# Kernel optimization log

Hardware: AMD Instinct MI355X
Metric: run time of the kernel (lower is better)

The kernel has to match this reference:

```python
import jax, jax.numpy as jnp
import numpy as np

FACTOR = 2  # upsample factor per spatial dim


def setup_inputs() -> dict:
    key = jax.random.key(0)
    k1, k2, k3 = jax.random.split(key, 3)
    B, C_in, C_out, H, W_ = 8, 128, 128, 64, 64
    x = jax.random.normal(k1, (B, C_in, H, W_), dtype=jnp.float32)
    # conv3x3 params (OIHW), fan-in scaled init like torch Conv2d default scale
    fan_in = C_in * 3 * 3
    W = jax.random.normal(k2, (C_out, C_in, 3, 3), dtype=jnp.float32) / np.sqrt(fan_in)
    b = jax.random.normal(k3, (C_out,), dtype=jnp.float32) * 0.01
    return {"x": x, "W": W, "b": b}


def reference(x, W, b):
    h = jnp.repeat(jnp.repeat(x, FACTOR, axis=2), FACTOR, axis=3)  # [B,C,2H,2W]
    # conv3x3: stride 1, padding 1
    out = jax.lax.conv_general_dilated(
        h, W,
        window_strides=(1, 1),
        padding=((1, 1), (1, 1)),
        dimension_numbers=("NCHW", "OIHW", "NCHW"),
    )
    return out + b[None, :, None, None]
```

## Files before the change

kernel.cpp:

```cpp
#include <hip/hip_runtime.h>
#include <stdint.h>

typedef short bf16x8 __attribute__((ext_vector_type(8)));
typedef float f32x4 __attribute__((ext_vector_type(4)));

#define NCI 128
#define NCO 128
#define HIN 64
#define HP  66
#define NB  8

__device__ __forceinline__ unsigned short f32_to_bf16(float f) {
    union { float f; uint32_t u; } v; v.f = f;
    return (unsigned short)((v.u + 0x7FFFu + ((v.u >> 16) & 1u)) >> 16);
}

__device__ __forceinline__ void gl_lds16(const void* g, void* l) {
    __builtin_amdgcn_global_load_lds(
        (const __attribute__((address_space(1))) unsigned int*)g,
        (__attribute__((address_space(3))) unsigned int*)l, 16, 0, 0);
}

__device__ __forceinline__ void vmw0() {
    asm volatile("s_waitcnt vmcnt(0)" ::: "memory");
}
__device__ __forceinline__ void lkw0() {
    asm volatile("s_waitcnt lgkmcnt(0)" ::: "memory");
}
__device__ __forceinline__ void barx() {
    asm volatile("" ::: "memory");
    __builtin_amdgcn_s_barrier();
    asm volatile("" ::: "memory");
}

__device__ __forceinline__ float weff_sum(const float* wp, int py, int px, int ty, int tx) {
    float s = 0.f;
    #pragma unroll
    for (int ky = 0; ky < 3; ++ky) {
        bool iy = (py == 0) ? (ty == 0 ? (ky == 0) : (ky >= 1))
                            : (ty == 0 ? (ky <= 1) : (ky == 2));
        if (!iy) continue;
        #pragma unroll
        for (int kx = 0; kx < 3; ++kx) {
            bool ix = (px == 0) ? (tx == 0 ? (kx == 0) : (kx >= 1))
                                : (tx == 0 ? (kx <= 1) : (kx == 2));
            if (ix) s += wp[ky * 3 + kx];
        }
    }
    return s;
}

__global__ __launch_bounds__(256) void prep_kernel(
        const float* __restrict__ W, const float* __restrict__ x,
        unsigned short* __restrict__ Aw5, unsigned short* __restrict__ xq) {
    if (blockIdx.x < 1024) {
        int idx = blockIdx.x * 256 + threadIdx.x;
        int e   = idx & 7;
        int rl  = (idx >> 3) & 15;
        int pl  = (idx >> 7) & 3;
        int f   = (idx >> 9) & 3;
        int wm  = (idx >> 11) & 1;
        int kt  = (idx >> 12) & 15;
        int par = idx >> 16;
        int co = wm * 64 + f * 16 + rl;
        int k  = kt * 32 + pl * 8 + e;
        int tap = k >> 7, ci = k & 127;
        Aw5[idx] = f32_to_bf16(weff_sum(W + (co * NCI + ci) * 9,
                                        par >> 1, par & 1, tap >> 1, tap & 1));
    } else {
        const int bb = blockIdx.x - 1024;
        const int b = bb / HP, hp = bb % HP;
        const int t = threadIdx.x;
        if (hp == 0 || hp == HP - 1) {
            bf16x8 z = (bf16x8){0, 0, 0, 0, 0, 0, 0, 0};
            for (int i = t; i < 4 * HP * 4; i += 256) {
                int g = i / (HP * 4), rem = i % (HP * 4);
                unsigned short* dst = xq +
                    ((((size_t)(b * 4 + g) * HP + hp) * HP) << 5) + rem * 8;
                *(bf16x8*)dst = z;
            }
            return;
        }
        const int h = hp - 1;
        if (t < 32) {
            bf16x8 z = (bf16x8){0, 0, 0, 0, 0, 0, 0, 0};
            int g = t >> 3, wpc = ((t >> 2) & 1) * (HP - 1), q = t & 3;
            unsigned short* dst = xq +
                ((((size_t)(b * 4 + g) * HP + hp) * HP + wpc) << 5) + q * 8;
            *(bf16x8*)dst = z;
        }
        const int w = t & 63, g = t >> 6;
        const float* src = x + ((size_t)(b * NCI + g * 32) * (HIN * HIN)) + h * HIN + w;
        unsigned short* dst = xq +
            ((((size_t)(b * 4 + g) * HP + hp) * HP + (w + 1)) << 5);
        #pragma unroll
        for (int q = 0; q < 4; ++q) {
            bf16x8 v;
            #pragma unroll
            for (int j = 0; j < 8; ++j)
                v[j] = (short)f32_to_bf16(src[(size_t)(q * 8 + j) * (HIN * HIN)]);
            *(bf16x8*)(dst + q * 8) = v;
        }
    }
}

__global__ __launch_bounds__(512, 4) void upconv10_kernel(
        const unsigned short* __restrict__ xq, const unsigned short* __restrict__ Aw5,
        const float* __restrict__ bv, float* __restrict__ out) {
    __shared__ __align__(16) unsigned short smem[25344];
    const int d = blockIdx.x;
    const int dsw = (d & 7) * 64 + (d >> 3);
    const int tile = dsw >> 1, py = dsw & 1;
    const int bi = tile >> 5;
    const int oy0 = (tile & 31) * 2;
    const int tid = threadIdx.x, lane = tid & 63, wv = tid >> 6;
    const int pxw = wv & 1, wm = (wv >> 1) & 1, wn = wv >> 2;
    const int rl = lane & 15, pl = lane >> 4;
    const int par = py * 2 + pxw;

    #pragma unroll
    for (int i = 0; i < 7; ++i) {
        int dd = i * 512 + tid;
        if (dd < 3168) {
            int cell = dd >> 4, chq = dd & 15;
            int ry = cell / 66, colg = cell - ry * 66;
            int chunk = chq ^ (colg & 15);
            const unsigned short* gb = xq +
                ((((size_t)(bi * 4 + (chunk >> 2)) * HP + (oy0 + py + ry)) * HP + colg) << 5)
                + (chunk & 3) * 8;
            gl_lds16(gb, &smem[dd * 8]);
        }
    }

    f32x4 acc[4][4];
    #pragma unroll
    for (int i = 0; i < 4; ++i)
        #pragma unroll
        for (int j = 0; j < 4; ++j)
            acc[i][j] = (f32x4){0.f, 0.f, 0.f, 0.f};

    bf16x8 A0[4], A1[4];
    auto loadA = [&](bf16x8* Ad, int kt2) {
        const unsigned short* p = Aw5 + (((par * 16 + kt2) * 2 + wm) << 11) + lane * 8;
        #pragma unroll
        for (int f = 0; f < 4; ++f)
            Ad[f] = *(const bf16x8*)(p + f * 512);
    };

    loadA(A0, 0);
    vmw0();
    barx();

    #pragma unroll 2
    for (int kt = 0; kt < 16; ++kt) {
        if (kt < 15) loadA((kt & 1) ? A0 : A1, kt + 1);
        const bf16x8* Ac = (kt & 1) ? A1 : A0;
        const int ty = kt >> 3, tx = (kt >> 2) & 1, cq = kt & 3;
        const int ry = wn + ty;
        __builtin_amdgcn_s_setprio(1);
        #pragma unroll
        for (int f = 0; f < 4; ++f) {
            const int colg = f * 16 + rl + pxw + tx;
            const int chq = (cq * 4 + pl) ^ (colg & 15);
            bf16x8 bfr = *(const bf16x8*)&smem[(((ry * 66 + colg) << 4) + chq) * 8];
            #pragma unroll
            for (int fm = 0; fm < 4; ++fm)
                acc[fm][f] = __builtin_amdgcn_mfma_f32_16x16x32_bf16(
                    Ac[fm], bfr, acc[fm][f], 0, 0, 0);
        }
        __builtin_amdgcn_s_setprio(0);
    }

    barx();

    float* lf = (float*)smem;
    const int co_l = tid >> 4;
    const int rem = tid & 15, rr = rem >> 3, x16 = (rem & 7) * 16;
    const int co_g = (co_l >> 4) * 64 + (co_l & 15);
    const int yy = 2 * (oy0 + rr) + py;

    #pragma unroll
    for (int fm = 0; fm < 4; ++fm) {
        #pragma unroll
        for (int fn = 0; fn < 4; ++fn) {
            int n = wn * 64 + fn * 16 + rl;
            int r = n >> 6, xx = 2 * (n & 63) + pxw;
            #pragma unroll
            for (int j = 0; j < 4; ++j) {
                int col = wm * 16 + pl * 4 + j;
                lf[col * 264 + r * 132 + xx] = acc[fm][fn][j];
            }
        }
        lkw0();
        barx();
        const int co = co_g + fm * 16;
        const float bb = bv[co];
        float* op = out + (((size_t)bi * NCO + co) * 128 + yy) * 128 + x16;
        const float* sp = lf + co_l * 264 + rr * 132 + x16;
        #pragma unroll
        for (int q = 0; q < 4; ++q) {
            f32x4 v = *(const f32x4*)(sp + q * 4);
            v[0] += bb; v[1] += bb; v[2] += bb; v[3] += bb;
            *(f32x4*)(op + q * 4) = v;
        }
        if (fm < 3) barx();
    }
}

__global__ void weff_flat_kernel(const float* __restrict__ W,
                                 unsigned short* __restrict__ Aw) {
    int idx = blockIdx.x * 256 + threadIdx.x;
    int par = idx >> 16;
    int co  = (idx >> 9) & 127;
    int k   = idx & 511;
    int tap = k >> 7, ci = k & 127;
    Aw[idx] = f32_to_bf16(weff_sum(W + (co * NCI + ci) * 9,
                                   par >> 1, par & 1, tap >> 1, tap & 1));
}

__global__ __launch_bounds__(256) void upconv_fb_kernel(
        const float* __restrict__ x, const unsigned short* __restrict__ Aw,
        const float* __restrict__ bv, float* __restrict__ out) {
    __shared__ __align__(16) unsigned short A_lds[128 * 32];
    __shared__ __align__(16) unsigned short B_lds[128 * 32];
    const int par = blockIdx.y, py = par >> 1, px = par & 1;
    const int s0 = blockIdx.x * 128;
    const int bimg = s0 >> 12;
    const int oy0 = (s0 >> 6) & 63;
    const int tid = threadIdx.x;
    const int lane = tid & 63, wave = tid >> 6;
    const int wm = wave >> 1, wn = wave & 1;
    const float* xb = x + bimg * (NCI * HIN * HIN);
    f32x4 acc[4][4];
    #pragma unroll
    for (int i = 0; i < 4; ++i)
        #pragma unroll
        for (int j = 0; j < 4; ++j)
            acc[i][j] = (f32x4){0.f, 0.f, 0.f, 0.f};
    for (int kt = 0; kt < 16; ++kt) {
        const int tap = kt >> 2, ci0 = (kt & 3) * 32;
        const int ty = tap >> 1, tx = tap & 1;
        #pragma unroll
        for (int i = 0; i < 2; ++i) {
            int c = i * 256 + tid;
            *(bf16x8*)(&A_lds[c * 8]) = *(const bf16x8*)(Aw +
                ((par * 128 + (c >> 2)) * 512 + kt * 32 + (c & 3) * 8));
        }
        #pragma unroll
        for (int i = 0; i < 2; ++i) {
            int tsk = i * 256 + tid;
            int n = tsk & 127, kg = tsk >> 7;
            int r = n >> 6, ox = n & 63;
            int row = oy0 + r - 1 + py + ty;
            int col = ox - 1 + px + tx;
            bool ok = (row >= 0) & (row < HIN) & (col >= 0) & (col < HIN);
            const float* xp = xb + (((ci0 + kg * 8) * HIN + row) * HIN + col);
            bf16x8 v;
            #pragma unroll
            for (int q = 0; q < 8; ++q) {
                float f = ok ? xp[q * (HIN * HIN)] : 0.f;
                v[q] = (short)f32_to_bf16(f);
            }
            *(bf16x8*)(&B_lds[n * 32 + kg * 8]) = v;
        }
        __syncthreads();
        const int seg = (lane >> 4) * 8, rl2 = lane & 15;
        bf16x8 af[4], bfr[4];
        #pragma unroll
        for (int f = 0; f < 4; ++f)
            af[f] = *(const bf16x8*)(&A_lds[(wm * 64 + f * 16 + rl2) * 32 + seg]);
        #pragma unroll
        for (int f = 0; f < 4; ++f)
            bfr[f] = *(const bf16x8*)(&B_lds[(wn * 64 + f * 16 + rl2) * 32 + seg]);
        #pragma unroll
        for (int fm = 0; fm < 4; ++fm)
            #pragma unroll
            for (int fn = 0; fn < 4; ++fn)
                acc[fm][fn] = __builtin_amdgcn_mfma_f32_16x16x32_bf16(
                    af[fm], bfr[fn], acc[fm][fn], 0, 0, 0);
        __syncthreads();
    }
    #pragma unroll
    for (int fm = 0; fm < 4; ++fm) {
        const int co_b = wm * 64 + fm * 16 + (lane >> 4) * 4;
        float bias4[4];
        #pragma unroll
        for (int j = 0; j < 4; ++j) bias4[j] = bv[co_b + j];
        #pragma unroll
        for (int fn = 0; fn < 4; ++fn) {
            int n = wn * 64 + fn * 16 + (lane & 15);
            int s = s0 + n;
            int ox = s & 63, oy = (s >> 6) & 63, bi2 = s >> 12;
            int yy = 2 * oy + py, xx = 2 * ox + px;
            float* op = out + ((size_t)bi2 * 128 * 128 * 128) + (size_t)yy * 128 + xx;
            #pragma unroll
            for (int j = 0; j < 4; ++j)
                op[(size_t)(co_b + j) * (128 * 128)] = acc[fm][fn][j] + bias4[j];
        }
    }
}

extern "C" void kernel_launch(void* const* d_in, const int* in_sizes, int n_in,
                              void* d_out, int out_size, void* d_ws, size_t ws_size,
                              hipStream_t stream) {
    const float* x  = (const float*)d_in[0];
    const float* W  = (const float*)d_in[1];
    const float* bv = (const float*)d_in[2];
    float* out = (float*)d_out;
    unsigned short* Aw = (unsigned short*)d_ws;
    const size_t aw_bytes = (size_t)4 * 16 * 2 * 2048 * sizeof(unsigned short);
    const size_t xq_bytes = (size_t)NB * 4 * HP * HP * 32 * sizeof(unsigned short);

    if (ws_size >= aw_bytes + xq_bytes) {
        unsigned short* xq = (unsigned short*)((char*)d_ws + aw_bytes);
        prep_kernel<<<1024 + NB * HP, 256, 0, stream>>>(W, x, Aw, xq);
        upconv10_kernel<<<512, 512, 0, stream>>>(xq, Aw, bv, out);
    } else {
        weff_flat_kernel<<<1024, 256, 0, stream>>>(W, Aw);
        upconv_fb_kernel<<<dim3(256, 4), 256, 0, stream>>>(x, Aw, bv, out);
    }
}
```

Before: 48.11 us.

## Halve block to 4 waves with each wave covering both output rows

The conv kernel now runs 256 threads (4 waves) per block instead of 8. Each wave computes a 64x128 tile, with 32 accumulators covering both output rows, rather than a 64x64 tile. This doubles reuse of the weight A-fragments loaded from global per MFMA and halves redundant A loads. The cost is more accumulator registers per thread, fewer waves to hide latency, and longer LDS staging and epilogue loops per thread.

```diff
diff --git a/kernel.cpp b/kernel.cpp
--- a/kernel.cpp
+++ b/kernel.cpp
@@ -104,7 +104,7 @@
     }
 }
 
-__global__ __launch_bounds__(512, 4) void upconv10_kernel(
+__global__ __launch_bounds__(256, 2) void upconv11_kernel(
         const unsigned short* __restrict__ xq, const unsigned short* __restrict__ Aw5,
         const float* __restrict__ bv, float* __restrict__ out) {
     __shared__ __align__(16) unsigned short smem[25344];
@@ -114,13 +114,13 @@
     const int bi = tile >> 5;
     const int oy0 = (tile & 31) * 2;
     const int tid = threadIdx.x, lane = tid & 63, wv = tid >> 6;
-    const int pxw = wv & 1, wm = (wv >> 1) & 1, wn = wv >> 2;
+    const int pxw = wv & 1, wm = wv >> 1;
     const int rl = lane & 15, pl = lane >> 4;
     const int par = py * 2 + pxw;
 
     #pragma unroll
-    for (int i = 0; i < 7; ++i) {
-        int dd = i * 512 + tid;
+    for (int i = 0; i < 13; ++i) {
+        int dd = i * 256 + tid;
         if (dd < 3168) {
             int cell = dd >> 4, chq = dd & 15;
             int ry = cell / 66, colg = cell - ry * 66;
@@ -132,11 +132,11 @@
         }
     }
 
-    f32x4 acc[4][4];
+    f32x4 acc[4][8];
     #pragma unroll
     for (int i = 0; i < 4; ++i)
         #pragma unroll
-        for (int j = 0; j < 4; ++j)
+        for (int j = 0; j < 8; ++j)
             acc[i][j] = (f32x4){0.f, 0.f, 0.f, 0.f};
 
     bf16x8 A0[4], A1[4];
@@ -156,11 +156,11 @@
         if (kt < 15) loadA((kt & 1) ? A0 : A1, kt + 1);
         const bf16x8* Ac = (kt & 1) ? A1 : A0;
         const int ty = kt >> 3, tx = (kt >> 2) & 1, cq = kt & 3;
-        const int ry = wn + ty;
         __builtin_amdgcn_s_setprio(1);
         #pragma unroll
-        for (int f = 0; f < 4; ++f) {
-            const int colg = f * 16 + rl + pxw + tx;
+        for (int f = 0; f < 8; ++f) {
+            const int ry = (f >> 2) + ty;
+            const int colg = (f & 3) * 16 + rl + pxw + tx;
             const int chq = (cq * 4 + pl) ^ (colg & 15);
             bf16x8 bfr = *(const bf16x8*)&smem[(((ry * 66 + colg) << 4) + chq) * 8];
             #pragma unroll
@@ -174,36 +174,40 @@
     barx();
 
     float* lf = (float*)smem;
-    const int co_l = tid >> 4;
-    const int rem = tid & 15, rr = rem >> 3, x16 = (rem & 7) * 16;
-    const int co_g = (co_l >> 4) * 64 + (co_l & 15);
+    const int co_l = tid >> 3;
+    const int rem = tid & 7, rr = rem >> 2, x32 = (rem & 3) * 32;
     const int yy = 2 * (oy0 + rr) + py;
 
     #pragma unroll
-    for (int fm = 0; fm < 4; ++fm) {
-        #pragma unroll
-        for (int fn = 0; fn < 4; ++fn) {
-            int n = wn * 64 + fn * 16 + rl;
-            int r = n >> 6, xx = 2 * (n & 63) + pxw;
-            #pragma unroll
-            for (int j = 0; j < 4; ++j) {
-                int col = wm * 16 + pl * 4 + j;
-                lf[col * 264 + r * 132 + xx] = acc[fm][fn][j];
+    for (int b = 0; b < 4; ++b) {
+        if (wm == (b >> 1)) {
+            const int fmb = (b & 1) * 2;
+            #pragma unroll
+            for (int f2 = 0; f2 < 2; ++f2) {
+                const int fm = fmb + f2;
+                #pragma unroll
+                for (int fn = 0; fn < 8; ++fn) {
+                    int n = fn * 16 + rl;
+                    int r = n >> 6, xx = 2 * (n & 63) + pxw;
+                    #pragma unroll
+                    for (int j = 0; j < 4; ++j)
+                        lf[(f2 * 16 + pl * 4 + j) * 264 + r * 132 + xx] = acc[fm][fn][j];
+                }
             }
         }
         lkw0();
         barx();
-        const int co = co_g + fm * 16;
+        const int co = b * 32 + co_l;
         const float bb = bv[co];
-        float* op = out + (((size_t)bi * NCO + co) * 128 + yy) * 128 + x16;
-        const float* sp = lf + co_l * 264 + rr * 132 + x16;
-        #pragma unroll
-        for (int q = 0; q < 4; ++q) {
+        float* op = out + (((size_t)bi * NCO + co) * 128 + yy) * 128 + x32;
+        const float* sp = lf + co_l * 264 + rr * 132 + x32;
+        #pragma unroll
+        for (int q = 0; q < 8; ++q) {
             f32x4 v = *(const f32x4*)(sp + q * 4);
             v[0] += bb; v[1] += bb; v[2] += bb; v[3] += bb;
             *(f32x4*)(op + q * 4) = v;
         }
-        if (fm < 3) barx();
+        if (b < 3) barx();
     }
 }
 
@@ -314,7 +318,7 @@
     if (ws_size >= aw_bytes + xq_bytes) {
         unsigned short* xq = (unsigned short*)((char*)d_ws + aw_bytes);
         prep_kernel<<<1024 + NB * HP, 256, 0, stream>>>(W, x, Aw, xq);
-        upconv10_kernel<<<512, 512, 0, stream>>>(xq, Aw, bv, out);
+        upconv11_kernel<<<512, 256, 0, stream>>>(xq, Aw, bv, out);
     } else {
         weff_flat_kernel<<<1024, 256, 0, stream>>>(W, Aw);
         upconv_fb_kernel<<<dim3(256, 4), 256, 0, stream>>>(x, Aw, bv, out);
```

Result: no change. 47.36 us (-1.5%).

## Drop LDS staging; load B fragments directly from global with register double-buffering

Applied to the files above, without the earlier changes.

The conv kernel no longer stages the padded input tile in LDS. Each wave now loads its B fragments straight from global/L2 into registers, double-buffered across k-steps with explicit vmcnt waits, and uses smaller 256-thread blocks covering one output row each. The epilogue writes accumulators directly to global with scattered stride-2 stores instead of transposing through LDS. This removes LDS traffic and barriers and should raise occupancy, at the cost of redundant global reads and poorly coalesced output stores.

```diff
diff --git a/kernel.cpp b/kernel.cpp
--- a/kernel.cpp
+++ b/kernel.cpp
@@ -13,24 +13,6 @@
 __device__ __forceinline__ unsigned short f32_to_bf16(float f) {
     union { float f; uint32_t u; } v; v.f = f;
     return (unsigned short)((v.u + 0x7FFFu + ((v.u >> 16) & 1u)) >> 16);
-}
-
-__device__ __forceinline__ void gl_lds16(const void* g, void* l) {
-    __builtin_amdgcn_global_load_lds(
-        (const __attribute__((address_space(1))) unsigned int*)g,
-        (__attribute__((address_space(3))) unsigned int*)l, 16, 0, 0);
-}
-
-__device__ __forceinline__ void vmw0() {
-    asm volatile("s_waitcnt vmcnt(0)" ::: "memory");
-}
-__device__ __forceinline__ void lkw0() {
-    asm volatile("s_waitcnt lgkmcnt(0)" ::: "memory");
-}
-__device__ __forceinline__ void barx() {
-    asm volatile("" ::: "memory");
-    __builtin_amdgcn_s_barrier();
-    asm volatile("" ::: "memory");
 }
 
 __device__ __forceinline__ float weff_sum(const float* wp, int py, int px, int ty, int tx) {
@@ -104,33 +86,23 @@
     }
 }
 
-__global__ __launch_bounds__(512, 4) void upconv10_kernel(
+__global__ __launch_bounds__(256, 4) void upconv12_kernel(
         const unsigned short* __restrict__ xq, const unsigned short* __restrict__ Aw5,
         const float* __restrict__ bv, float* __restrict__ out) {
-    __shared__ __align__(16) unsigned short smem[25344];
     const int d = blockIdx.x;
-    const int dsw = (d & 7) * 64 + (d >> 3);
-    const int tile = dsw >> 1, py = dsw & 1;
-    const int bi = tile >> 5;
-    const int oy0 = (tile & 31) * 2;
+    const int dsw = (d & 7) * 128 + (d >> 3);
+    const int py = dsw & 1;
+    const int t = dsw >> 1;
+    const int bi = t >> 6;
+    const int oy0 = t & 63;
     const int tid = threadIdx.x, lane = tid & 63, wv = tid >> 6;
-    const int pxw = wv & 1, wm = (wv >> 1) & 1, wn = wv >> 2;
+    const int pxw = wv & 1, wm = wv >> 1;
     const int rl = lane & 15, pl = lane >> 4;
     const int par = py * 2 + pxw;
 
-    #pragma unroll
-    for (int i = 0; i < 7; ++i) {
-        int dd = i * 512 + tid;
-        if (dd < 3168) {
-            int cell = dd >> 4, chq = dd & 15;
-            int ry = cell / 66, colg = cell - ry * 66;
-            int chunk = chq ^ (colg & 15);
-            const unsigned short* gb = xq +
-                ((((size_t)(bi * 4 + (chunk >> 2)) * HP + (oy0 + py + ry)) * HP + colg) << 5)
-                + (chunk & 3) * 8;
-            gl_lds16(gb, &smem[dd * 8]);
-        }
-    }
+    const unsigned short* Ab = Aw5 + ((par * 16 * 2 + wm) << 11) + lane * 8;
+    const char* xqb = (const char*)xq + (((size_t)bi * 4 * HP * HP) << 6);
+    const int blane = rl * 64 + pl * 16;
 
     f32x4 acc[4][4];
     #pragma unroll
@@ -139,71 +111,67 @@
         for (int j = 0; j < 4; ++j)
             acc[i][j] = (f32x4){0.f, 0.f, 0.f, 0.f};
 
-    bf16x8 A0[4], A1[4];
-    auto loadA = [&](bf16x8* Ad, int kt2) {
-        const unsigned short* p = Aw5 + (((par * 16 + kt2) * 2 + wm) << 11) + lane * 8;
+    bf16x8 A0[4], B0[4], B1[4];
+
+    auto loadA = [&](int kt) {
+        const unsigned short* p = Ab + (kt << 12);
         #pragma unroll
         for (int f = 0; f < 4; ++f)
-            Ad[f] = *(const bf16x8*)(p + f * 512);
+            A0[f] = *(const bf16x8*)(p + f * 512);
     };
-
-    loadA(A0, 0);
-    vmw0();
-    barx();
-
-    #pragma unroll 2
-    for (int kt = 0; kt < 16; ++kt) {
-        if (kt < 15) loadA((kt & 1) ? A0 : A1, kt + 1);
-        const bf16x8* Ac = (kt & 1) ? A1 : A0;
-        const int ty = kt >> 3, tx = (kt >> 2) & 1, cq = kt & 3;
-        const int ry = wn + ty;
-        __builtin_amdgcn_s_setprio(1);
-        #pragma unroll
-        for (int f = 0; f < 4; ++f) {
-            const int colg = f * 16 + rl + pxw + tx;
-            const int chq = (cq * 4 + pl) ^ (colg & 15);
-            bf16x8 bfr = *(const bf16x8*)&smem[(((ry * 66 + colg) << 4) + chq) * 8];
-            #pragma unroll
-            for (int fm = 0; fm < 4; ++fm)
-                acc[fm][f] = __builtin_amdgcn_mfma_f32_16x16x32_bf16(
-                    Ac[fm], bfr, acc[fm][f], 0, 0, 0);
-        }
+    auto loadB = [&](bf16x8* Bd, int kt) {
+        const int row = oy0 + py + (kt >> 3);
+        const int g = kt & 3;
+        const int cb = pxw + ((kt >> 2) & 1);
+        const char* base = xqb + (((g * HP + row) * HP + cb) << 6) + blane;
+        #pragma unroll
+        for (int fn = 0; fn < 4; ++fn)
+            Bd[fn] = *(const bf16x8*)(base + fn * 1024);
+    };
+
+    #define MFMA_STEP(BB)                                                     \
+        __builtin_amdgcn_s_setprio(1);                                        \
+        _Pragma("unroll")                                                     \
+        for (int fn = 0; fn < 4; ++fn) {                                      \
+            _Pragma("unroll")                                                 \
+            for (int fm = 0; fm < 4; ++fm)                                    \
+                acc[fm][fn] = __builtin_amdgcn_mfma_f32_16x16x32_bf16(        \
+                    A0[fm], BB[fn], acc[fm][fn], 0, 0, 0);                    \
+        }                                                                     \
         __builtin_amdgcn_s_setprio(0);
-    }
-
-    barx();
-
-    float* lf = (float*)smem;
-    const int co_l = tid >> 4;
-    const int rem = tid & 15, rr = rem >> 3, x16 = (rem & 7) * 16;
-    const int co_g = (co_l >> 4) * 64 + (co_l & 15);
-    const int yy = 2 * (oy0 + rr) + py;
-
+
+    loadB(B0, 0);
+    for (int kp = 0; kp < 8; ++kp) {
+        int kt = kp * 2;
+        loadA(kt);
+        loadB(B1, kt + 1);
+        asm volatile("s_waitcnt vmcnt(4)" ::: "memory");
+        MFMA_STEP(B0)
+        kt = kp * 2 + 1;
+        loadA(kt);
+        if (kp < 7) {
+            loadB(B0, kt + 1);
+            asm volatile("s_waitcnt vmcnt(4)" ::: "memory");
+        } else {
+            asm volatile("s_waitcnt vmcnt(0)" ::: "memory");
+        }
+        MFMA_STEP(B1)
+    }
+    #undef MFMA_STEP
+
+    const int yy = 2 * oy0 + py;
+    float* ob = out + (((size_t)bi * NCO + wm * 64 + pl * 4) << 14)
+                    + yy * 128 + 2 * rl + pxw;
     #pragma unroll
     for (int fm = 0; fm < 4; ++fm) {
         #pragma unroll
-        for (int fn = 0; fn < 4; ++fn) {
-            int n = wn * 64 + fn * 16 + rl;
-            int r = n >> 6, xx = 2 * (n & 63) + pxw;
-            #pragma unroll
-            for (int j = 0; j < 4; ++j) {
-                int col = wm * 16 + pl * 4 + j;
-                lf[col * 264 + r * 132 + xx] = acc[fm][fn][j];
-            }
-        }
-        lkw0();
-        barx();
-        const int co = co_g + fm * 16;
-        const float bb = bv[co];
-        float* op = out + (((size_t)bi * NCO + co) * 128 + yy) * 128 + x16;
-        const float* sp = lf + co_l * 264 + rr * 132 + x16;
-        #pragma unroll
-        for (int q = 0; q < 4; ++q) {
-            f32x4 v = *(const f32x4*)(sp + q * 4);
-            v[0] += bb; v[1] += bb; v[2] += bb; v[3] += bb;
-            *(f32x4*)(op + q * 4) = v;
-        }
-        if (fm < 3) barx();
+        for (int j = 0; j < 4; ++j) {
+            const float bb = bv[wm * 64 + fm * 16 + pl * 4 + j];
+            float* o2 = ob + ((fm * 16 + j) << 14);
+            #pragma unroll
+            for (int fn = 0; fn < 4; ++fn)
+                o2[fn * 32] = acc[fm][fn][j] + bb;
+        }
     }
 }
 
@@ -314,7 +282,7 @@
     if (ws_size >= aw_bytes + xq_bytes) {
         unsigned short* xq = (unsigned short*)((char*)d_ws + aw_bytes);
         prep_kernel<<<1024 + NB * HP, 256, 0, stream>>>(W, x, Aw, xq);
-        upconv10_kernel<<<512, 512, 0, stream>>>(xq, Aw, bv, out);
+        upconv12_kernel<<<1024, 256, 0, stream>>>(xq, Aw, bv, out);
     } else {
         weff_flat_kernel<<<1024, 256, 0, stream>>>(W, Aw);
         upconv_fb_kernel<<<dim3(256, 4), 256, 0, stream>>>(x, Aw, bv, out);
```

Measured after the change: 47.16 us. 2.0% less time.
